# Performance work log

Measured on AMD Instinct MI355X. Metric: run time of the kernel, lower is better.

The kernel has to match this reference:

```python
import jax, jax.numpy as jnp
import numpy as np

ORIENTATIONS = 9
CELL = 8  # pixels_per_cell


def setup_inputs() -> dict:
    key = jax.random.key(0)
    x = jax.random.normal(key, (64, 1, 512, 512), dtype=jnp.float32)
    base = jnp.array([[1.0, 0.0, -1.0], [2.0, 0.0, -2.0], [1.0, 0.0, -1.0]], dtype=jnp.float32)
    weight = jnp.stack([base, base.T])[:, None, :, :]  # [2,1,3,3]
    return {"x": x, "weight": weight}


def reference(x, weight):
    # 3x3 Sobel-like gradient conv (cross-correlation, padding=1), NCHW
    gxy = jax.lax.conv_general_dilated(
        x, weight, window_strides=(1, 1), padding=[(1, 1), (1, 1)],
        dimension_numbers=("NCHW", "OIHW", "NCHW"))  # [n,2,h,w]
    gx, gy = gxy[:, 0], gxy[:, 1]
    mag = jnp.sqrt(gx * gx + gy * gy)            # [n,h,w]
    phase = jnp.arctan2(gx, gy)                  # [n,h,w]
    phase_int = phase / jnp.pi * ORIENTATIONS
    fl = jnp.floor(phase_int).astype(jnp.int32) % ORIENTATIONS
    ce = jnp.ceil(phase_int).astype(jnp.int32) % ORIENTATIONS
    # scatter_(set into zeros) + scatter_add_ == sum of two weighted one-hots
    hist = (jax.nn.one_hot(fl, ORIENTATIONS, dtype=mag.dtype)
            + jax.nn.one_hot(ce, ORIENTATIONS, dtype=mag.dtype)) * mag[..., None]  # [n,h,w,O]
    out = jnp.transpose(hist, (0, 3, 1, 2))      # [n,O,h,w]
    n, o, h, w = out.shape
    # avg_pool2d with kernel==stride==CELL
    pooled = out.reshape(n, o, h // CELL, CELL, w // CELL, CELL).mean(axis=(3, 5))
    return pooled.reshape(n, -1)  # feature_vector=True
```

## Files before the change

### kernel.cpp

```cpp
#include <hip/hip_runtime.h>
#include <math.h>


#define IMH 512
#define IMW 512

#define F32(h) __builtin_bit_cast(float, (unsigned)(h))
__device__ __forceinline__ unsigned fbits(float f) { return __builtin_bit_cast(unsigned, f); }
__device__ __forceinline__ int mod9(int b) { int r = b % 9; return r < 0 ? r + 9 : r; }

__device__ float fd_atanf_fma(float x) {
#pragma clang fp contract(off)
    unsigned hx = fbits(x);
    unsigned ix = hx & 0x7fffffffu;
    if (ix >= 0x4c800000u) {
        if (ix > 0x7f800000u) return x + x;
        float r = F32(0x3fc90fda) + F32(0x33a22168);
        return (hx >> 31) ? -r : r;
    }
    int id;
    if (ix < 0x3ee00000u) {
        if (ix < 0x39800000u) return x;
        id = -1;
    } else {
        x = fabsf(x);
        if (ix < 0x3f980000u) {
            if (ix < 0x3f300000u) { id = 0; x = fmaf(2.0f, x, -1.0f) / (2.0f + x); }
            else                  { id = 1; x = (x - 1.0f) / (x + 1.0f); }
        } else {
            if (ix < 0x401c0000u) { id = 2; x = (x - 1.5f) / fmaf(1.5f, x, 1.0f); }
            else                  { id = 3; x = -1.0f / x; }
        }
    }
    float z = x * x;
    float w = z * z;
    float s1 = z * fmaf(w, fmaf(w, F32(0x3d7cac25), F32(0x3e11f50d)), F32(0x3eaaaaa3));
    float s2 = w * fmaf(w, F32(0xbdda1247), F32(0xbe4cca98));
    if (id < 0) return fmaf(-x, s1 + s2, x);
    float hi = (id == 0) ? F32(0x3eed6338) : (id == 1) ? F32(0x3f490fda)
             : (id == 2) ? F32(0x3f7b985e) : F32(0x3fc90fda);
    float lo = (id == 0) ? F32(0x31ac3769) : (id == 1) ? F32(0x33222168)
             : (id == 2) ? F32(0x33140fb4) : F32(0x33a22168);
    float zz = hi - (fmaf(x, s1 + s2, -lo) - x);
    return (hx >> 31) ? -zz : zz;
}

__device__ float fd_atan2f_fma(float y, float x) {
#pragma clang fp contract(off)
    unsigned hx = fbits(x), hy = fbits(y);
    unsigned ix = hx & 0x7fffffffu, iy = hy & 0x7fffffffu;
    const float pi     = F32(0x40490fdb);
    const float pi_lo  = F32(0xb3bbbd2e);
    const float pi_o_2 = F32(0x3fc90fdb);
    if (hx == 0x3f800000u) return fd_atanf_fma(y);
    unsigned m = ((hy >> 31) & 1u) | ((hx >> 30) & 2u);
    if (iy == 0u) {
        switch (m) {
            case 0: case 1: return y;
            case 2: return pi;
            default: return -pi;
        }
    }
    if (ix == 0u) return (hy >> 31) ? -pi_o_2 : pi_o_2;
    int k = ((int)iy - (int)ix) >> 23;
    float z;
    unsigned mm = m;
    if (k > 26) {
        z = pi_o_2 + 0.5f * pi_lo;
        mm = m & 1u;
    } else if (k < -26 && (hx >> 31)) {
        z = 0.0f;
    } else {
        z = fd_atanf_fma(fabsf(y / x));
    }
    switch (mm) {
        case 0:  return z;
        case 1:  return -z;
        case 2:  return pi - (z - pi_lo);
        default: return (z - pi_lo) - pi;
    }
}

__global__ __launch_bounds__(256) void hog_kernel(const float* __restrict__ x,
                                                  float* __restrict__ out) {
#pragma clang fp contract(off)
    const int tid  = threadIdx.x;
    const int wid  = tid >> 6;
    const int lane = tid & 63;
    const int bid  = blockIdx.x;
    const int n  = bid >> 7;
    const int ch = (bid >> 1) & 63;
    const int sb = bid & 1;
    const int r  = lane >> 3;
    const int c  = lane & 7;
    const int cw = sb * 32 + wid * 8 + c;
    const int h  = (ch << 3) + r;
    const int wpx0 = cw << 3;

    const float* xn = x + (size_t)n * (IMH * IMW);
    const int hm = h - 1, hp = h + 1;
    const bool rok0 = (hm >= 0), rok2 = (hp < IMH);
    const float* rowm = xn + (size_t)(rok0 ? hm : 0) * IMW;
    const float* row0 = xn + (size_t)h * IMW;
    const float* rowp = xn + (size_t)(rok2 ? hp : 0) * IMW;

    float a0, a1, b0, b1, cc0, cc1;
    {
        int cm1 = wpx0 - 1;
        bool cok = (cm1 >= 0);
        a0  = (rok0 && cok) ? rowm[cm1] : 0.0f;
        b0  = cok ? row0[cm1] : 0.0f;
        cc0 = (rok2 && cok) ? rowp[cm1] : 0.0f;
        a1  = rok0 ? rowm[wpx0] : 0.0f;
        b1  = row0[wpx0];
        cc1 = rok2 ? rowp[wpx0] : 0.0f;
    }

    float hreg[9];
#pragma unroll
    for (int o = 0; o < 9; ++o) hreg[o] = 0.0f;

    for (int px = 0; px < 8; ++px) {
        int col = wpx0 + px + 1;
        bool cok = (col < IMW);
        float a2  = (rok0 && cok) ? rowm[col] : 0.0f;
        float b2  = cok ? row0[col] : 0.0f;
        float cc2 = (rok2 && cok) ? rowp[col] : 0.0f;

        float gx = a0;
        gx = gx - a2;
        gx = gx + 2.0f * b0;
        gx = gx - 2.0f * b2;
        gx = gx + cc0;
        gx = gx - cc2;

        float gy = a0;
        gy = gy + 2.0f * a1;
        gy = gy + a2;
        gy = gy - cc0;
        gy = gy - 2.0f * cc1;
        gy = gy - cc2;

        float m2f = gx * gx + gy * gy;
        float mag = sqrtf(m2f);

        float Sx = fabsf(a0) + fabsf(a2)
                 + 2.0f * (fabsf(b0) + fabsf(b2))
                 + fabsf(cc0) + fabsf(cc2);
        float Sy = fabsf(a0) + fabsf(cc0)
                 + 2.0f * (fabsf(a1) + fabsf(cc1))
                 + fabsf(a2) + fabsf(cc2);

        float ph32 = atan2f(gx, gy);
        float t32 = (ph32 / F32(0x40490fdb)) * 9.0f;
        float agx = fabsf(gx), agy = fabsf(gy);
        float Eph32 = 3.0e-7f * fabsf(ph32) + 1e-12f;
        if (m2f > 0.0f)
            Eph32 += (agy * (3.6e-7f * Sx) + agx * (3.6e-7f * Sy)) / m2f;
        float Et32 = 2.8648f * Eph32 + 3.6e-7f * fmaxf(fabsf(t32), 1.0f)
                   + 3.5e-8f * fabsf(t32);
        float d32 = fabsf(t32 - rintf(t32));

        int bn0 = 0, bn1 = 0, bn2 = 0;
        float wt0 = 0.0f, wt1 = 0.0f, wt2 = 0.0f;

        if (d32 > 4.0f * Et32 && m2f > 0.0f) {
            int k0 = (int)floorf(t32);
            bn0 = mod9(k0); bn1 = mod9(k0 + 1);
            wt0 = mag; wt1 = mag;
        } else {
            double gx64 = ((double)a0 - (double)a2)
                        + 2.0 * ((double)b0 - (double)b2)
                        + ((double)cc0 - (double)cc2);
            double gy64 = ((double)a0 - (double)cc0)
                        + 2.0 * ((double)a1 - (double)cc1)
                        + ((double)a2 - (double)cc2);
            double m2 = gx64 * gx64 + gy64 * gy64;
            if (m2 == 0.0) {
                bn0 = 0; bn1 = 0; wt0 = mag; wt1 = mag;
            } else {
                double ph = atan2(gx64, gy64);
                double t64 = (ph / 3.14159274101257324) * 9.0;
                double dgx = 2.4e-7 * (double)Sx;
                double dgy = 2.4e-7 * (double)Sy;
                double dpa = (fabs(gy64) * dgx + fabs(gx64) * dgy) / m2;
                double dpi = 2.4e-7 * fabs(ph) + 1e-30;
                double E = 2.86479 * (dpa + dpi)
                         + 1.8e-7 * fmax(fabs(t64), 1.0)
                         + 3.5e-8 * fabs(t64);
                double kd = floor(t64 + 0.5);
                double d = fabs(t64 - kd);
                int k = (int)kd;
                if (d <= E) {
                    if (mag <= 8.3f) {
                        bn0 = mod9(k - 1); bn1 = mod9(k); bn2 = mod9(k + 1);
                        wt0 = 0.5f * mag; wt1 = 1.5f * mag; wt2 = 0.5f * mag;
                    } else {
                        float phf = fd_atan2f_fma(gx, gy);
                        float tf = (phf / F32(0x40490fdb)) * 9.0f;
                        int fl = (int)floorf(tf);
                        int ce = (int)ceilf(tf);
                        bn0 = mod9(fl); bn1 = mod9(ce);
                        wt0 = mag; wt1 = mag;
                    }
                } else {
                    int k0 = (int)floor(t64);
                    bn0 = mod9(k0); bn1 = mod9(k0 + 1);
                    wt0 = mag; wt1 = mag;
                }
            }
        }

#pragma unroll
        for (int o = 0; o < 9; ++o)
            hreg[o] += (bn0 == o ? wt0 : 0.0f) + (bn1 == o ? wt1 : 0.0f)
                     + (bn2 == o ? wt2 : 0.0f);

        a0 = a1; a1 = a2;
        b0 = b1; b1 = b2;
        cc0 = cc1; cc1 = cc2;
    }

#pragma unroll
    for (int o = 0; o < 9; ++o) {
        float s = hreg[o];
        s += __shfl_xor(s, 8, 64);
        s += __shfl_xor(s, 16, 64);
        s += __shfl_xor(s, 32, 64);
        hreg[o] = s;
    }

    float val = hreg[0];
#pragma unroll
    for (int o = 1; o < 8; ++o) val = (r == o) ? hreg[o] : val;
    out[(((size_t)n * 9 + r) * 64 + ch) * 64 + cw] = val * (1.0f / 64.0f);
    if (r == 0)
        out[(((size_t)n * 9 + 8) * 64 + ch) * 64 + cw] = hreg[8] * (1.0f / 64.0f);
}

extern "C" void kernel_launch(void* const* d_in, const int* in_sizes, int n_in,
                              void* d_out, int out_size, void* d_ws, size_t ws_size,
                              hipStream_t stream) {
    const float* x = (const float*)d_in[0];
    float* out = (float*)d_out;
    const int blocks = 64 * 64 * 2;
    hog_kernel<<<blocks, 256, 0, stream>>>(x, out);
}
```

Measured before the change: 195.0 us.

## Replace atan2f with polynomial approximation, outline slow path, and use LDS histograms

Swaps the library atan2f on the fast path for a short minimax polynomial atan with octant fixups, and rewrites the error-bound test as a division-free comparison with a wider margin. The double-precision fallback moves into a noinline function so the hot loop stays small and uses fewer registers. Per-thread histograms now live in shared memory and are updated by bin index, replacing the 9-way select-accumulate, and the pixel loop is fully unrolled. The risks are a larger share of pixels taking the slow path because of the coarser polynomial, a function call inside a divergent branch, and the cost of LDS read-modify-write traffic.

```diff
diff --git a/kernel.cpp b/kernel.cpp
--- a/kernel.cpp
+++ b/kernel.cpp
@@ -81,9 +81,56 @@
     }
 }
 
+__device__ __attribute__((noinline)) void slow_bins(
+    float a0, float a1, float a2, float b0, float b2,
+    float cc0, float cc1, float cc2,
+    float gx, float gy, float mag, float Sx, float Sy,
+    int& bn0, int& bn1, int& bn2, float& wt0, float& wt1, float& wt2)
+{
+#pragma clang fp contract(off)
+    bn0 = 0; bn1 = 0; bn2 = 0;
+    wt0 = mag; wt1 = mag; wt2 = 0.0f;
+    double gx64 = ((double)a0 - (double)a2)
+                + 2.0 * ((double)b0 - (double)b2)
+                + ((double)cc0 - (double)cc2);
+    double gy64 = ((double)a0 - (double)cc0)
+                + 2.0 * ((double)a1 - (double)cc1)
+                + ((double)a2 - (double)cc2);
+    double m2 = gx64 * gx64 + gy64 * gy64;
+    if (m2 == 0.0) return;
+    double ph = atan2(gx64, gy64);
+    double t64 = (ph / 3.14159274101257324) * 9.0;
+    double dgx = 2.4e-7 * (double)Sx;
+    double dgy = 2.4e-7 * (double)Sy;
+    double dpa = (fabs(gy64) * dgx + fabs(gx64) * dgy) / m2;
+    double dpi = 2.4e-7 * fabs(ph) + 1e-30;
+    double E = 2.86479 * (dpa + dpi)
+             + 1.8e-7 * fmax(fabs(t64), 1.0)
+             + 3.5e-8 * fabs(t64);
+    double kd = floor(t64 + 0.5);
+    double d = fabs(t64 - kd);
+    int k = (int)kd;
+    if (d <= E) {
+        if (mag <= 8.3f) {
+            bn0 = mod9(k - 1); bn1 = mod9(k); bn2 = mod9(k + 1);
+            wt0 = 0.5f * mag; wt1 = 1.5f * mag; wt2 = 0.5f * mag;
+        } else {
+            float phf = fd_atan2f_fma(gx, gy);
+            float tf = (phf / F32(0x40490fdb)) * 9.0f;
+            int fl = (int)floorf(tf);
+            int ce = (int)ceilf(tf);
+            bn0 = mod9(fl); bn1 = mod9(ce);
+        }
+    } else {
+        int k0 = (int)floor(t64);
+        bn0 = mod9(k0); bn1 = mod9(k0 + 1);
+    }
+}
+
 __global__ __launch_bounds__(256) void hog_kernel(const float* __restrict__ x,
                                                   float* __restrict__ out) {
-#pragma clang fp contract(off)
+    __shared__ float hist[256 * 9];
+
     const int tid  = threadIdx.x;
     const int wid  = tid >> 6;
     const int lane = tid & 63;
@@ -98,11 +145,15 @@
     const int wpx0 = cw << 3;
 
     const float* xn = x + (size_t)n * (IMH * IMW);
-    const int hm = h - 1, hp = h + 1;
-    const bool rok0 = (hm >= 0), rok2 = (hp < IMH);
+    const int hm = h - 1, hpr = h + 1;
+    const bool rok0 = (hm >= 0), rok2 = (hpr < IMH);
     const float* rowm = xn + (size_t)(rok0 ? hm : 0) * IMW;
     const float* row0 = xn + (size_t)h * IMW;
-    const float* rowp = xn + (size_t)(rok2 ? hp : 0) * IMW;
+    const float* rowp = xn + (size_t)(rok2 ? hpr : 0) * IMW;
+
+    float* hp9 = &hist[tid * 9];
+#pragma unroll
+    for (int o = 0; o < 9; ++o) hp9[o] = 0.0f;
 
     float a0, a1, b0, b1, cc0, cc1;
     {
@@ -116,10 +167,7 @@
         cc1 = rok2 ? rowp[wpx0] : 0.0f;
     }
 
-    float hreg[9];
-#pragma unroll
-    for (int o = 0; o < 9; ++o) hreg[o] = 0.0f;
-
+#pragma unroll
     for (int px = 0; px < 8; ++px) {
         int col = wpx0 + px + 1;
         bool cok = (col < IMW);
@@ -127,19 +175,23 @@
         float b2  = cok ? row0[col] : 0.0f;
         float cc2 = (rok2 && cok) ? rowp[col] : 0.0f;
 
-        float gx = a0;
-        gx = gx - a2;
-        gx = gx + 2.0f * b0;
-        gx = gx - 2.0f * b2;
-        gx = gx + cc0;
-        gx = gx - cc2;
-
-        float gy = a0;
-        gy = gy + 2.0f * a1;
-        gy = gy + a2;
-        gy = gy - cc0;
-        gy = gy - 2.0f * cc1;
-        gy = gy - cc2;
+        float gx, gy;
+        {
+#pragma clang fp contract(off)
+            gx = a0;
+            gx = gx - a2;
+            gx = gx + 2.0f * b0;
+            gx = gx - 2.0f * b2;
+            gx = gx + cc0;
+            gx = gx - cc2;
+
+            gy = a0;
+            gy = gy + 2.0f * a1;
+            gy = gy + a2;
+            gy = gy - cc0;
+            gy = gy - 2.0f * cc1;
+            gy = gy - cc2;
+        }
 
         float m2f = gx * gx + gy * gy;
         float mag = sqrtf(m2f);
@@ -151,76 +203,47 @@
                  + 2.0f * (fabsf(a1) + fabsf(cc1))
                  + fabsf(a2) + fabsf(cc2);
 
-        float ph32 = atan2f(gx, gy);
-        float t32 = (ph32 / F32(0x40490fdb)) * 9.0f;
         float agx = fabsf(gx), agy = fabsf(gy);
-        float Eph32 = 3.0e-7f * fabsf(ph32) + 1e-12f;
-        if (m2f > 0.0f)
-            Eph32 += (agy * (3.6e-7f * Sx) + agx * (3.6e-7f * Sy)) / m2f;
-        float Et32 = 2.8648f * Eph32 + 3.6e-7f * fmaxf(fabsf(t32), 1.0f)
-                   + 3.5e-8f * fabsf(t32);
+        float hi = fmaxf(agx, agy), lo = fminf(agx, agy);
+        float rr = __fdividef(lo, hi);
+        float r2 = rr * rr;
+        float p = fmaf(r2, 0.0208351f, -0.0851330f);
+        p = fmaf(r2, p, 0.1801410f);
+        p = fmaf(r2, p, -0.3302995f);
+        p = fmaf(r2, p, 0.9998660f);
+        float base = rr * p;
+        float th = (agx > agy) ? (1.57079637f - base) : base;
+        th = (gy < 0.0f) ? (3.14159274f - th) : th;
+        th = copysignf(th, gx);
+        float t32 = th * 2.86478901f;
         float d32 = fabsf(t32 - rintf(t32));
 
-        int bn0 = 0, bn1 = 0, bn2 = 0;
-        float wt0 = 0.0f, wt1 = 0.0f, wt2 = 0.0f;
-
-        if (d32 > 4.0f * Et32 && m2f > 0.0f) {
+        float u = fmaf(agy, Sx, agx * Sy);
+        bool fast = (d32 * m2f > fmaf(8.0e-4f, m2f, 4.126e-6f * u)) && (m2f > 0.0f);
+
+        int bn0, bn1, bn2 = 0;
+        float wt0, wt1, wt2 = 0.0f;
+        if (fast) {
             int k0 = (int)floorf(t32);
             bn0 = mod9(k0); bn1 = mod9(k0 + 1);
             wt0 = mag; wt1 = mag;
         } else {
-            double gx64 = ((double)a0 - (double)a2)
-                        + 2.0 * ((double)b0 - (double)b2)
-                        + ((double)cc0 - (double)cc2);
-            double gy64 = ((double)a0 - (double)cc0)
-                        + 2.0 * ((double)a1 - (double)cc1)
-                        + ((double)a2 - (double)cc2);
-            double m2 = gx64 * gx64 + gy64 * gy64;
-            if (m2 == 0.0) {
-                bn0 = 0; bn1 = 0; wt0 = mag; wt1 = mag;
-            } else {
-                double ph = atan2(gx64, gy64);
-                double t64 = (ph / 3.14159274101257324) * 9.0;
-                double dgx = 2.4e-7 * (double)Sx;
-                double dgy = 2.4e-7 * (double)Sy;
-                double dpa = (fabs(gy64) * dgx + fabs(gx64) * dgy) / m2;
-                double dpi = 2.4e-7 * fabs(ph) + 1e-30;
-                double E = 2.86479 * (dpa + dpi)
-                         + 1.8e-7 * fmax(fabs(t64), 1.0)
-                         + 3.5e-8 * fabs(t64);
-                double kd = floor(t64 + 0.5);
-                double d = fabs(t64 - kd);
-                int k = (int)kd;
-                if (d <= E) {
-                    if (mag <= 8.3f) {
-                        bn0 = mod9(k - 1); bn1 = mod9(k); bn2 = mod9(k + 1);
-                        wt0 = 0.5f * mag; wt1 = 1.5f * mag; wt2 = 0.5f * mag;
-                    } else {
-                        float phf = fd_atan2f_fma(gx, gy);
-                        float tf = (phf / F32(0x40490fdb)) * 9.0f;
-                        int fl = (int)floorf(tf);
-                        int ce = (int)ceilf(tf);
-                        bn0 = mod9(fl); bn1 = mod9(ce);
-                        wt0 = mag; wt1 = mag;
-                    }
-                } else {
-                    int k0 = (int)floor(t64);
-                    bn0 = mod9(k0); bn1 = mod9(k0 + 1);
-                    wt0 = mag; wt1 = mag;
-                }
-            }
-        }
-
-#pragma unroll
-        for (int o = 0; o < 9; ++o)
-            hreg[o] += (bn0 == o ? wt0 : 0.0f) + (bn1 == o ? wt1 : 0.0f)
-                     + (bn2 == o ? wt2 : 0.0f);
+            slow_bins(a0, a1, a2, b0, b2, cc0, cc1, cc2,
+                      gx, gy, mag, Sx, Sy, bn0, bn1, bn2, wt0, wt1, wt2);
+        }
+
+        hp9[bn0] += wt0;
+        hp9[bn1] += wt1;
+        if (wt2 != 0.0f) hp9[bn2] += wt2;
 
         a0 = a1; a1 = a2;
         b0 = b1; b1 = b2;
         cc0 = cc1; cc1 = cc2;
     }
 
+    float hreg[9];
+#pragma unroll
+    for (int o = 0; o < 9; ++o) hreg[o] = hp9[o];
 #pragma unroll
     for (int o = 0; o < 9; ++o) {
         float s = hreg[o];
```

Measured after the change: 202.5 us. 1.04x slower.
